# Performance work log

Measured on AMD Instinct MI355X. Metric: run time of the kernel, lower is better.

Reference implementation:

```python
import jax, jax.numpy as jnp
import numpy as np

N_HEAD = 16
THETA = 10000.0


def _freqs_cos_sin(head_dim, seq_len):
    # matches precompute_freqs_cis: freqs = 1/theta^(arange(0,dim,2)/dim), outer with t
    inv = 1.0 / (THETA ** (jnp.arange(0, head_dim, 2, dtype=jnp.float32) / head_dim))
    t = jnp.arange(seq_len, dtype=jnp.float32)
    ang = jnp.outer(t, inv)  # [L, head_dim//2]
    return jnp.cos(ang), jnp.sin(ang)


def _rope(x, cos, sin):
    # x: [B, H, L, D]; pairs are interleaved (view_as_complex on (..., D//2, 2))
    x1 = x[..., 0::2]
    x2 = x[..., 1::2]
    out_re = x1 * cos - x2 * sin
    out_im = x1 * sin + x2 * cos
    return jnp.stack([out_re, out_im], axis=-1).reshape(x.shape)


def setup_inputs() -> dict:
    key = jax.random.key(0)
    ks = jax.random.split(key, 11)
    B, L, D = 2, 2048, 1024
    s = 0.02
    return {
        "q": jax.random.normal(ks[0], (B, L, D), jnp.float32),
        "k": jax.random.normal(ks[1], (B, L, D), jnp.float32),
        "v": jax.random.normal(ks[2], (B, L, D), jnp.float32),
        "wq": jax.random.normal(ks[3], (D, D), jnp.float32) * s,
        "bq": jax.random.normal(ks[4], (D,), jnp.float32) * s,
        "wk": jax.random.normal(ks[5], (D, D), jnp.float32) * s,
        "bk": jax.random.normal(ks[6], (D,), jnp.float32) * s,
        "wv": jax.random.normal(ks[7], (D, D), jnp.float32) * s,
        "bv": jax.random.normal(ks[8], (D,), jnp.float32) * s,
        "wo": jax.random.normal(ks[9], (D, D), jnp.float32) * s,
        "bo": jax.random.normal(ks[10], (D,), jnp.float32) * s,
    }


def reference(q, k, v, wq, bq, wk, bk, wv, bv, wo, bo):
    B, L, D = q.shape
    Hd = D // N_HEAD
    # projections (nn.Linear: x @ W^T + b)
    qp = q @ wq.T + bq
    kp = k @ wk.T + bk
    vp = v @ wv.T + bv
    # split: [B, L, D] -> [B, H, L, Hd]
    def split(t):
        return t.reshape(B, L, N_HEAD, Hd).transpose(0, 2, 1, 3)
    qh, kh, vh = split(qp), split(kp), split(vp)
    cos, sin = _freqs_cos_sin(Hd, L)  # [L, Hd//2], broadcasts over B, H
    qh = _rope(qh, cos, sin)
    kh = _rope(kh, cos, sin)
    # scaled dot-product attention (no mask)
    scores = jnp.einsum("bhqd,bhkd->bhqk", qh, kh) / jnp.sqrt(jnp.float32(Hd))
    attn = jax.nn.softmax(scores, axis=-1)
    out = jnp.einsum("bhqk,bhkd->bhqd", attn, vh)
    # concat heads and output projection
    out = out.transpose(0, 2, 1, 3).reshape(B, L, D)
    return out @ wo.T + bo
```

## Files before the change

kernel.cpp:

```cpp
#include <hip/hip_runtime.h>
#include <hip/hip_bf16.h>
#include <math.h>

#define BB 2
#define LL 2048
#define DD 1024
#define NH 16
#define HD 64

typedef short v8s __attribute__((ext_vector_type(8)));
typedef float v4f __attribute__((ext_vector_type(4)));
typedef float v16f __attribute__((ext_vector_type(16)));

__device__ __forceinline__ float b2f(unsigned short b) {
  union { unsigned int u; float f; } c; c.u = ((unsigned int)b) << 16; return c.f;
}
__device__ __forceinline__ unsigned short f2b(float x) {
  union { float f; unsigned int u; } c; c.f = x;
  unsigned int u = c.u;
  u += 0x7fffu + ((u >> 16) & 1u);
  return (unsigned short)(u >> 16);
}
__device__ __forceinline__ unsigned int asu(float x) {
  union { float f; unsigned int u; } c; c.f = x; return c.u;
}
__device__ __forceinline__ unsigned int pk2(float lo, float hi) {
  return __builtin_amdgcn_perm(asu(hi), asu(lo), 0x07060302u);
}

#if defined(__has_builtin)
#if __has_builtin(__builtin_amdgcn_exp2f)
#define EXP2(x) __builtin_amdgcn_exp2f(x)
#else
#define EXP2(x) __expf((x) * 0.69314718056f)
#endif
#else
#define EXP2(x) __expf((x) * 0.69314718056f)
#endif

__device__ __forceinline__ void gload16(const void* g, void* l) {
  __builtin_amdgcn_global_load_lds(
      (const __attribute__((address_space(1))) void*)g,
      (__attribute__((address_space(3))) void*)l, 16, 0, 0);
}

#define VM_WAIT4 do { asm volatile("s_waitcnt vmcnt(4)" ::: "memory"); \
                      __builtin_amdgcn_sched_barrier(0); } while (0)
#define VM_WAIT2 do { asm volatile("s_waitcnt vmcnt(2)" ::: "memory"); \
                      __builtin_amdgcn_sched_barrier(0); } while (0)
#define VM_WAIT0 do { asm volatile("s_waitcnt vmcnt(0)" ::: "memory"); \
                      __builtin_amdgcn_sched_barrier(0); } while (0)
#define SBAR     do { __builtin_amdgcn_s_barrier(); \
                      __builtin_amdgcn_sched_barrier(0); } while (0)

struct CastArgs { const float* s[7]; unsigned short* d[7]; float* ct; float* st; };
__global__ void cast_all(CastArgs a) {
  int z = blockIdx.z;
  if (z == 16) {
    if (blockIdx.x >= 256) return;
    int id = blockIdx.x * blockDim.x + threadIdx.x;
    int t = id >> 5, i = id & 31;
    float inv = powf(10000.0f, -(float)(2 * i) / 64.0f);
    float ang = (float)t * inv;
    a.ct[id] = cosf(ang);
    a.st[id] = sinf(ang);
    return;
  }
  int t = (z < 12) ? (z >> 2) : (z - 9);
  int off = (z < 12) ? ((z & 3) << 18) : 0;
  int i = off + blockIdx.x * blockDim.x + threadIdx.x;
  float4 v = ((const float4*)a.s[t])[i];
  ushort4 o;
  o.x = f2b(v.x); o.y = f2b(v.y); o.z = f2b(v.z); o.w = f2b(v.w);
  ((ushort4*)a.d[t])[i] = o;
}

__device__ __forceinline__ size_t ring_src_off(int id, int row0, int Kd) {
  int sr = id >> 3, slot = id & 7;
  int g = slot ^ (sr & 7);
  int r = (sr << 1) | (g >> 2), c = g & 3;
  return (size_t)(row0 + r) * Kd + c * 8;
}
__device__ __forceinline__ int ring_frag_off(int row, int quad) {
  int sr = row >> 1;
  int slot = (((row & 1) << 2) | quad) ^ (sr & 7);
  return sr * 64 + slot * 8;
}

__device__ __forceinline__ void ring_gemm_core(
    const unsigned short* __restrict__ X, const unsigned short* __restrict__ W,
    unsigned short* LDS_, int bm0, int bn0, v4f acc[4][4]) {
  const int K = DD;
  const int tid = threadIdx.x;
  const int lane = tid & 63, wave = tid >> 6;
  const int quad = lane >> 4, l16 = lane & 15;
  const int wm = (wave >> 1) * 64, wn = (wave & 1) * 64;

  const unsigned short* aS0 = X + ring_src_off(tid, bm0, K);
  const unsigned short* aS1 = X + ring_src_off(256 + tid, bm0, K);
  const unsigned short* bS0 = W + ring_src_off(tid, bn0, K);
  const unsigned short* bS1 = W + ring_src_off(256 + tid, bn0, K);

  int aoff[4], boff[4];
#pragma unroll
  for (int i = 0; i < 4; ++i) {
    aoff[i] = ring_frag_off(wm + i * 16 + l16, quad);
    boff[i] = ring_frag_off(wn + i * 16 + l16, quad);
  }

  auto stage = [&](int q, int kofs) {
    unsigned short* Ab = &LDS_[q * 4096];
    unsigned short* Bb = &LDS_[12288 + q * 4096];
    gload16(aS0 + kofs, &Ab[tid * 8]);
    gload16(aS1 + kofs, &Ab[(256 + tid) * 8]);
    gload16(bS0 + kofs, &Bb[tid * 8]);
    gload16(bS1 + kofs, &Bb[(256 + tid) * 8]);
  };
  auto compute = [&](int q) {
    const unsigned short* Ab = &LDS_[q * 4096];
    const unsigned short* Bb = &LDS_[12288 + q * 4096];
    v8s a[4], b[4];
#pragma unroll
    for (int i = 0; i < 4; ++i) {
      a[i] = *(const v8s*)&Ab[aoff[i]];
      b[i] = *(const v8s*)&Bb[boff[i]];
    }
#pragma unroll
    for (int mi = 0; mi < 4; ++mi)
#pragma unroll
      for (int ni = 0; ni < 4; ++ni)
        acc[mi][ni] = __builtin_amdgcn_mfma_f32_16x16x32_bf16(a[mi], b[ni], acc[mi][ni], 0, 0, 0);
  };

  const int nt = K / 32;
  stage(0, 0);
  stage(1, 32);
  VM_WAIT4;
  SBAR;
  int cur = 0, s2 = 2, kofs = 64;
#pragma unroll 1
  for (int t = 0; t < nt - 2; ++t) {
    stage(s2, kofs);
    compute(cur);
    VM_WAIT4;
    SBAR;
    cur = (cur == 2) ? 0 : cur + 1;
    s2 = (s2 == 2) ? 0 : s2 + 1;
    kofs += 32;
  }
  compute(cur);
  VM_WAIT0;
  SBAR;
  cur = (cur == 2) ? 0 : cur + 1;
  compute(cur);
}

__global__ __launch_bounds__(256, 3) void gemm_qkv(
    const unsigned short* __restrict__ qb, const unsigned short* __restrict__ kb,
    const unsigned short* __restrict__ vb,
    const unsigned short* __restrict__ wqb, const unsigned short* __restrict__ wkb,
    const unsigned short* __restrict__ wvb,
    const float* __restrict__ bq, const float* __restrict__ bk,
    const float* __restrict__ bv_,
    unsigned short* __restrict__ qp, unsigned short* __restrict__ khh,
    unsigned short* __restrict__ vt,
    const float* __restrict__ ctab, const float* __restrict__ stab) {
  __shared__ __align__(16) unsigned short LDS_[24576];
  const int z = blockIdx.z;
  const unsigned short* X = (z == 0) ? qb : (z == 1) ? kb : vb;
  const unsigned short* W = (z == 0) ? wqb : (z == 1) ? wkb : wvb;
  const float* bias = (z == 0) ? bq : (z == 1) ? bk : bv_;
  const int N = DD;
  const int tid = threadIdx.x;
  const int lane = tid & 63, wave = tid >> 6;
  const int quad = lane >> 4, l16 = lane & 15;
  const int bm0 = blockIdx.x * 128;
  const int bn0 = blockIdx.y * 128;
  const int wm = (wave >> 1) * 64, wn = (wave & 1) * 64;

  const v4f vzero = {0.f, 0.f, 0.f, 0.f};
  v4f acc[4][4];
#pragma unroll
  for (int i = 0; i < 4; ++i)
#pragma unroll
    for (int j = 0; j < 4; ++j) acc[i][j] = vzero;

  ring_gemm_core(X, W, LDS_, bm0, bn0, acc);

  float bv[4];
#pragma unroll
  for (int ni = 0; ni < 4; ++ni) bv[ni] = bias[bn0 + wn + ni * 16 + l16];

  if (z < 2) {
    const float scl = (z == 0) ? 0.18033688f : 1.0f;
    const int h = (bn0 + wn) >> 6;
    const float sgn = (l16 & 1) ? 1.0f : -1.0f;
#pragma unroll
    for (int mi = 0; mi < 4; ++mi) {
#pragma unroll
      for (int r = 0; r < 4; ++r) {
        int row = bm0 + wm + mi * 16 + quad * 4 + r;
        int l = row & (LL - 1);
        int bidx = row >> 11;
        size_t baseq = (size_t)row * N + bn0 + wn + l16;
        size_t basek = ((size_t)(bidx * NH + h) * LL + l) * HD + l16;
#pragma unroll
        for (int ni = 0; ni < 4; ++ni) {
          int ii = (ni * 16 + l16) >> 1;
          float c = ctab[l * 32 + ii], s = stab[l * 32 + ii];
          float v = acc[mi][ni][r] + bv[ni];
          float vp = __shfl_xor(v, 1);
          float o = (v * c + sgn * (vp * s)) * scl;
          if (z == 0) qp[baseq + ni * 16] = f2b(o);
          else        khh[basek + ni * 16] = f2b(o);
        }
      }
    }
  } else {
    __syncthreads();
    unsigned short* T = LDS_;
#pragma unroll
    for (int mi = 0; mi < 4; ++mi)
#pragma unroll
      for (int r = 0; r < 4; ++r) {
        int tl = wm + mi * 16 + quad * 4 + r;
        int tlp = (tl & ~12) | ((tl & 4) << 1) | ((tl & 8) >> 1);
        int chunk = tlp >> 3, offw = tlp & 7;
#pragma unroll
        for (int ni = 0; ni < 4; ++ni) {
          int fl = wn + ni * 16 + l16;
          T[fl * 128 + ((chunk ^ (fl & 15)) * 8) + offw] =
              f2b(acc[mi][ni][r] + bv[ni]);
        }
      }
    __syncthreads();
    int fl = tid >> 1, half = tid & 1;
    int fg = bn0 + fl;
    int h2 = fg >> 6, d = fg & 63;
    int bidx = bm0 >> 11, l0 = bm0 & (LL - 1);
    unsigned short* dst =
        vt + (((size_t)(bidx * NH + h2) * HD + d) * LL) + l0 + half * 64;
#pragma unroll
    for (int i = 0; i < 8; ++i) {
      int chunk = half * 8 + i;
      int slot = chunk ^ (fl & 15);
      *(v8s*)(dst + i * 8) = *(const v8s*)&T[fl * 128 + slot * 8];
    }
  }
}

__global__ __launch_bounds__(256, 3) void gemm_out(
    const unsigned short* __restrict__ x, const unsigned short* __restrict__ w,
    const float* __restrict__ b, float* __restrict__ y) {
  __shared__ __align__(16) unsigned short LDS_[24576];
  const int N = DD;
  const int tid = threadIdx.x;
  const int lane = tid & 63, wave = tid >> 6;
  const int quad = lane >> 4, l16 = lane & 15;
  const int bm0 = blockIdx.x * 128;
  const int bn0 = blockIdx.y * 128;
  const int wm = (wave >> 1) * 64, wn = (wave & 1) * 64;

  const v4f vzero = {0.f, 0.f, 0.f, 0.f};
  v4f acc[4][4];
#pragma unroll
  for (int i = 0; i < 4; ++i)
#pragma unroll
    for (int j = 0; j < 4; ++j) acc[i][j] = vzero;

  ring_gemm_core(x, w, LDS_, bm0, bn0, acc);

  float bv[4];
#pragma unroll
  for (int ni = 0; ni < 4; ++ni) bv[ni] = b[bn0 + wn + ni * 16 + l16];
#pragma unroll
  for (int mi = 0; mi < 4; ++mi) {
#pragma unroll
    for (int r = 0; r < 4; ++r) {
      int row = bm0 + wm + mi * 16 + quad * 4 + r;
      size_t base = (size_t)row * N + bn0 + wn + l16;
#pragma unroll
      for (int ni = 0; ni < 4; ++ni)
        y[base + ni * 16] = acc[mi][ni][r] + bv[ni];
    }
  }
}

__global__ __launch_bounds__(256, 4) void flash_split(
    const unsigned short* __restrict__ qp,
    const unsigned short* __restrict__ kh,
    const unsigned short* __restrict__ vt,
    unsigned short* __restrict__ opart,
    float* __restrict__ lspart) {
  __shared__ __align__(16) unsigned short S_[12288];
  const int tid = threadIdx.x, wave = tid >> 6, lane = tid & 63;
  const int l32 = lane & 31, hf = lane >> 5;
  const int bh = blockIdx.x, b = bh >> 4, hd = bh & 15;
  const int qt = blockIdx.y, ks = blockIdx.z;
  const int q0 = qt * 128;
  const unsigned short* kbase = kh + (size_t)bh * LL * HD + (size_t)ks * 1024 * HD;
  const unsigned short* vbase = vt + (size_t)bh * HD * LL + ks * 1024;

  const int qrow = q0 + wave * 32 + l32;
  v8s qf[4];
  {
    const unsigned short* qsrc = qp + ((size_t)(b * LL + qrow) * DD + hd * HD);
#pragma unroll
    for (int ks2 = 0; ks2 < 4; ++ks2)
      qf[ks2] = *(const v8s*)(qsrc + ks2 * 16 + hf * 8);
  }

  const int rk = tid >> 3, sk = tid & 7;
  const int rv = tid >> 2, sv = tid & 3;
  const unsigned short* kS = kbase + (size_t)rk * HD + ((sk ^ (rk & 7)) * 8);
  const unsigned short* vS = vbase + (size_t)rv * LL + ((sv ^ (rv & 3)) * 8);

  v16f o0, o1;
#pragma unroll
  for (int i = 0; i < 16; ++i) { o0[i] = 0.0f; o1[i] = 0.0f; }
  float ls = 0.0f;

  auto stage = [&](int q, int t) {
    gload16(kS + t * 2048, &S_[q * 4096 + tid * 8]);
    gload16(vS + t * 32, &S_[q * 4096 + 2048 + tid * 8]);
  };

  auto compute = [&](int q) {
    const unsigned short* Ks = &S_[q * 4096];
    const unsigned short* Vs = Ks + 2048;
    v16f sc;
#pragma unroll
    for (int i = 0; i < 16; ++i) sc[i] = 0.0f;
#pragma unroll
    for (int ks2 = 0; ks2 < 4; ++ks2) {
      v8s kf = *(const v8s*)&Ks[l32 * 64 + (((ks2 * 2 + hf) ^ (l32 & 7)) * 8)];
      sc = __builtin_amdgcn_mfma_f32_32x32x16_bf16(kf, qf[ks2], sc, 0, 0, 0);
    }
    v16f e;
#pragma unroll
    for (int i = 0; i < 16; ++i) e[i] = EXP2(sc[i]);
    float t0 = (e[0] + e[1]) + (e[2] + e[3]);
    float t1 = (e[4] + e[5]) + (e[6] + e[7]);
    float t2 = (e[8] + e[9]) + (e[10] + e[11]);
    float t3 = (e[12] + e[13]) + (e[14] + e[15]);
    ls += (t0 + t1) + (t2 + t3);
    union { v8s v; unsigned int u[4]; } pb0, pb1;
#pragma unroll
    for (int a = 0; a < 4; ++a) {
      pb0.u[a] = pk2(e[2 * a], e[2 * a + 1]);
      pb1.u[a] = pk2(e[8 + 2 * a], e[8 + 2 * a + 1]);
    }
    int slot0 = (hf) ^ (l32 & 3);
    int slot1 = (2 + hf) ^ (l32 & 3);
    v8s vfa0 = *(const v8s*)&Vs[l32 * 32 + slot0 * 8];
    v8s vfb0 = *(const v8s*)&Vs[(32 + l32) * 32 + slot0 * 8];
    v8s vfa1 = *(const v8s*)&Vs[l32 * 32 + slot1 * 8];
    v8s vfb1 = *(const v8s*)&Vs[(32 + l32) * 32 + slot1 * 8];
    o0 = __builtin_amdgcn_mfma_f32_32x32x16_bf16(vfa0, pb0.v, o0, 0, 0, 0);
    o1 = __builtin_amdgcn_mfma_f32_32x32x16_bf16(vfb0, pb0.v, o1, 0, 0, 0);
    o0 = __builtin_amdgcn_mfma_f32_32x32x16_bf16(vfa1, pb1.v, o0, 0, 0, 0);
    o1 = __builtin_amdgcn_mfma_f32_32x32x16_bf16(vfb1, pb1.v, o1, 0, 0, 0);
  };

  const int nt = 32;
  stage(0, 0);
  stage(1, 1);
  VM_WAIT2;
  SBAR;
  int cur = 0, s2 = 2;
#pragma unroll 1
  for (int t = 0; t < nt - 2; ++t) {
    stage(s2, t + 2);
    compute(cur);
    VM_WAIT2;
    SBAR;
    cur = (cur == 2) ? 0 : cur + 1;
    s2 = (s2 == 2) ? 0 : s2 + 1;
  }
  compute(cur);
  VM_WAIT0;
  SBAR;
  cur = (cur == 2) ? 0 : cur + 1;
  compute(cur);

  const int blk4 = ((bh * 16 + qt) * 2 + ks) * 4 + wave;
  lspart[blk4 * 64 + lane] = ls;
  unsigned short* ob = opart + (size_t)blk4 * 2048;
#pragma unroll
  for (int r = 0; r < 16; ++r) {
    ob[r * 64 + lane] = f2b(o0[r]);
    ob[(16 + r) * 64 + lane] = f2b(o1[r]);
  }
}

__global__ __launch_bounds__(256) void flash_combine(
    const unsigned short* __restrict__ opart, const float* __restrict__ lspart,
    unsigned short* __restrict__ attn) {
  __shared__ __align__(16) unsigned short W_[8192];
  const int tid = threadIdx.x, wave = tid >> 6, lane = tid & 63;
  const int l32 = lane & 31, hf = lane >> 5;
  const int bh = blockIdx.x, b = bh >> 4, hd = bh & 15;
  const int qt = blockIdx.y, q0 = qt * 128;

  const int p0 = ((bh * 16 + qt) * 2 + 0) * 4 + wave;
  const int p1 = p0 + 4;
  float lsv = lspart[p0 * 64 + lane] + lspart[p1 * 64 + lane];
  lsv += __shfl_xor(lsv, 32);
  float inv = 1.0f / lsv;

  const unsigned short* oa = opart + (size_t)p0 * 2048;
  const unsigned short* ob = opart + (size_t)p1 * 2048;
  unsigned short* Wt = W_ + wave * 2048;
#pragma unroll
  for (int dt = 0; dt < 2; ++dt)
#pragma unroll
    for (int r = 0; r < 16; ++r) {
      int idx = (dt * 16 + r) * 64 + lane;
      float val = (b2f(oa[idx]) + b2f(ob[idx])) * inv;
      int dl = (r & 3) + 8 * (r >> 2) + 4 * hf;
      int d = dt * 32 + dl;
      int chunk = d >> 3, offw = d & 7;
      int slot = chunk ^ (l32 & 7);
      Wt[l32 * 64 + slot * 8 + offw] = f2b(val);
    }
#pragma unroll
  for (int i = 0; i < 4; ++i) {
    int qr = lane >> 1;
    int chunk = (lane & 1) * 4 + i;
    int slot = chunk ^ (qr & 7);
    v8s dv = *(const v8s*)&Wt[qr * 64 + slot * 8];
    int token = q0 + wave * 32 + qr;
    *(v8s*)(attn + ((size_t)(b * LL + token) * DD) + hd * HD + chunk * 8) = dv;
  }
}

extern "C" void kernel_launch(void* const* d_in, const int* in_sizes, int n_in,
                              void* d_out, int out_size, void* d_ws, size_t ws_size,
                              hipStream_t stream) {
  const float* q  = (const float*)d_in[0];
  const float* k  = (const float*)d_in[1];
  const float* v  = (const float*)d_in[2];
  const float* wq = (const float*)d_in[3];
  const float* bq = (const float*)d_in[4];
  const float* wk = (const float*)d_in[5];
  const float* bk = (const float*)d_in[6];
  const float* wv = (const float*)d_in[7];
  const float* bv = (const float*)d_in[8];
  const float* wo = (const float*)d_in[9];
  const float* bo = (const float*)d_in[10];
  float* out = (float*)d_out;

  size_t off = 0;
  char* wsb = (char*)d_ws;
  auto take = [&](size_t n) { void* p = wsb + off; off += n; return p; };
  const size_t SZT = (size_t)BB * LL * DD * 2;
  const size_t SZW = (size_t)DD * DD * 2;
  unsigned short* qb   = (unsigned short*)take(SZT);
  unsigned short* kb   = (unsigned short*)take(SZT);
  unsigned short* vb   = (unsigned short*)take(SZT);
  unsigned short* wqb  = (unsigned short*)take(SZW);
  unsigned short* wkb  = (unsigned short*)take(SZW);
  unsigned short* wvb  = (unsigned short*)take(SZW);
  unsigned short* wob  = (unsigned short*)take(SZW);
  unsigned short* qp   = (unsigned short*)take(SZT);
  unsigned short* khh  = (unsigned short*)take(SZT);
  unsigned short* vtt  = (unsigned short*)take(SZT);
  unsigned short* attn = (unsigned short*)take(SZT);
  float* ctab = (float*)take((size_t)LL * 32 * 4);
  float* stab = (float*)take((size_t)LL * 32 * 4);

  unsigned short* opart = qb;
  float* lspart = (float*)wqb;

  CastArgs ca;
  ca.s[0] = q;  ca.s[1] = k;  ca.s[2] = v;  ca.s[3] = wq;
  ca.s[4] = wk; ca.s[5] = wv; ca.s[6] = wo;
  ca.d[0] = qb;  ca.d[1] = kb;  ca.d[2] = vb;  ca.d[3] = wqb;
  ca.d[4] = wkb; ca.d[5] = wvb; ca.d[6] = wob;
  ca.ct = ctab; ca.st = stab;
  cast_all<<<dim3(1024, 1, 17), 256, 0, stream>>>(ca);

  gemm_qkv<<<dim3(BB * LL / 128, DD / 128, 3), 256, 0, stream>>>(
      qb, kb, vb, wqb, wkb, wvb, bq, bk, bv, qp, khh, vtt, ctab, stab);

  flash_split<<<dim3(BB * NH, LL / 128, 2), 256, 0, stream>>>(
      qp, khh, vtt, opart, lspart);

  flash_combine<<<dim3(BB * NH, LL / 128), 256, 0, stream>>>(
      opart, lspart, attn);

  gemm_out<<<dim3(BB * LL / 128, DD / 128, 1), 256, 0, stream>>>(attn, wob, bo, out);
}
```

Before: 220.4 us.

## Process two 32-row query tiles per wave to reuse K/V LDS fragments

Each wave in the flash attention kernel now handles 64 query rows as two 32-row groups instead of 32. The K and V fragments read from LDS are reused across both groups, and the V staging layout and read offsets are rearranged. The grid is halved along the query dimension and the combine kernel is updated to match. The aim is to halve K/V global and LDS traffic per query row. The cost is roughly double the accumulator registers, lower occupancy (launch bounds drop from 4 to 2), and fewer blocks to fill the GPU.

```diff
diff --git a/kernel.cpp b/kernel.cpp
--- a/kernel.cpp
+++ b/kernel.cpp
@@ -286,7 +286,7 @@
   }
 }
 
-__global__ __launch_bounds__(256, 4) void flash_split(
+__global__ __launch_bounds__(256, 2) void flash_split(
     const unsigned short* __restrict__ qp,
     const unsigned short* __restrict__ kh,
     const unsigned short* __restrict__ vt,
@@ -297,69 +297,111 @@
   const int l32 = lane & 31, hf = lane >> 5;
   const int bh = blockIdx.x, b = bh >> 4, hd = bh & 15;
   const int qt = blockIdx.y, ks = blockIdx.z;
-  const int q0 = qt * 128;
+  const int qbase = qt * 256 + wave * 64;
   const unsigned short* kbase = kh + (size_t)bh * LL * HD + (size_t)ks * 1024 * HD;
   const unsigned short* vbase = vt + (size_t)bh * HD * LL + ks * 1024;
 
-  const int qrow = q0 + wave * 32 + l32;
-  v8s qf[4];
+  v8s qfA[4], qfB[4];
   {
-    const unsigned short* qsrc = qp + ((size_t)(b * LL + qrow) * DD + hd * HD);
-#pragma unroll
-    for (int ks2 = 0; ks2 < 4; ++ks2)
-      qf[ks2] = *(const v8s*)(qsrc + ks2 * 16 + hf * 8);
+    const unsigned short* qa = qp + ((size_t)(b * LL + qbase + l32) * DD + hd * HD);
+    const unsigned short* qbp = qp + ((size_t)(b * LL + qbase + 32 + l32) * DD + hd * HD);
+#pragma unroll
+    for (int ks2 = 0; ks2 < 4; ++ks2) {
+      qfA[ks2] = *(const v8s*)(qa + ks2 * 16 + hf * 8);
+      qfB[ks2] = *(const v8s*)(qbp + ks2 * 16 + hf * 8);
+    }
   }
 
   const int rk = tid >> 3, sk = tid & 7;
-  const int rv = tid >> 2, sv = tid & 3;
   const unsigned short* kS = kbase + (size_t)rk * HD + ((sk ^ (rk & 7)) * 8);
-  const unsigned short* vS = vbase + (size_t)rv * LL + ((sv ^ (rv & 3)) * 8);
-
-  v16f o0, o1;
-#pragma unroll
-  for (int i = 0; i < 16; ++i) { o0[i] = 0.0f; o1[i] = 0.0f; }
-  float ls = 0.0f;
+  const int srv = tid >> 3, slv = tid & 7;
+  const int gv = slv ^ (srv & 7);
+  const int dv_ = srv * 2 + (gv >> 2), cv = gv & 3;
+  const unsigned short* vS = vbase + (size_t)dv_ * LL + cv * 8;
+
+  v16f oA0, oA1, oB0, oB1;
+#pragma unroll
+  for (int i = 0; i < 16; ++i) { oA0[i] = 0.f; oA1[i] = 0.f; oB0[i] = 0.f; oB1[i] = 0.f; }
+  float lsA = 0.0f, lsB = 0.0f;
 
   auto stage = [&](int q, int t) {
     gload16(kS + t * 2048, &S_[q * 4096 + tid * 8]);
     gload16(vS + t * 32, &S_[q * 4096 + 2048 + tid * 8]);
   };
 
+  int voff[2][2];
+#pragma unroll
+  for (int k16 = 0; k16 < 2; ++k16) {
+    int c = k16 * 2 + hf;
+    int srA = l32 >> 1;
+    int srB = 16 + (l32 >> 1);
+    voff[k16][0] = srA * 64 + ((((l32 & 1) * 4 + c) ^ (srA & 7)) * 8);
+    voff[k16][1] = srB * 64 + ((((l32 & 1) * 4 + c) ^ (srB & 7)) * 8);
+  }
+  int koff[4];
+#pragma unroll
+  for (int ks2 = 0; ks2 < 4; ++ks2)
+    koff[ks2] = l32 * 64 + (((ks2 * 2 + hf) ^ (l32 & 7)) * 8);
+
   auto compute = [&](int q) {
     const unsigned short* Ks = &S_[q * 4096];
     const unsigned short* Vs = Ks + 2048;
+    v8s kf[4];
     v16f sc;
 #pragma unroll
     for (int i = 0; i < 16; ++i) sc[i] = 0.0f;
 #pragma unroll
     for (int ks2 = 0; ks2 < 4; ++ks2) {
-      v8s kf = *(const v8s*)&Ks[l32 * 64 + (((ks2 * 2 + hf) ^ (l32 & 7)) * 8)];
-      sc = __builtin_amdgcn_mfma_f32_32x32x16_bf16(kf, qf[ks2], sc, 0, 0, 0);
+      kf[ks2] = *(const v8s*)&Ks[koff[ks2]];
+      sc = __builtin_amdgcn_mfma_f32_32x32x16_bf16(kf[ks2], qfA[ks2], sc, 0, 0, 0);
     }
     v16f e;
 #pragma unroll
     for (int i = 0; i < 16; ++i) e[i] = EXP2(sc[i]);
-    float t0 = (e[0] + e[1]) + (e[2] + e[3]);
-    float t1 = (e[4] + e[5]) + (e[6] + e[7]);
-    float t2 = (e[8] + e[9]) + (e[10] + e[11]);
-    float t3 = (e[12] + e[13]) + (e[14] + e[15]);
-    ls += (t0 + t1) + (t2 + t3);
+    {
+      float t0 = (e[0] + e[1]) + (e[2] + e[3]);
+      float t1 = (e[4] + e[5]) + (e[6] + e[7]);
+      float t2 = (e[8] + e[9]) + (e[10] + e[11]);
+      float t3 = (e[12] + e[13]) + (e[14] + e[15]);
+      lsA += (t0 + t1) + (t2 + t3);
+    }
     union { v8s v; unsigned int u[4]; } pb0, pb1;
 #pragma unroll
     for (int a = 0; a < 4; ++a) {
       pb0.u[a] = pk2(e[2 * a], e[2 * a + 1]);
       pb1.u[a] = pk2(e[8 + 2 * a], e[8 + 2 * a + 1]);
     }
-    int slot0 = (hf) ^ (l32 & 3);
-    int slot1 = (2 + hf) ^ (l32 & 3);
-    v8s vfa0 = *(const v8s*)&Vs[l32 * 32 + slot0 * 8];
-    v8s vfb0 = *(const v8s*)&Vs[(32 + l32) * 32 + slot0 * 8];
-    v8s vfa1 = *(const v8s*)&Vs[l32 * 32 + slot1 * 8];
-    v8s vfb1 = *(const v8s*)&Vs[(32 + l32) * 32 + slot1 * 8];
-    o0 = __builtin_amdgcn_mfma_f32_32x32x16_bf16(vfa0, pb0.v, o0, 0, 0, 0);
-    o1 = __builtin_amdgcn_mfma_f32_32x32x16_bf16(vfb0, pb0.v, o1, 0, 0, 0);
-    o0 = __builtin_amdgcn_mfma_f32_32x32x16_bf16(vfa1, pb1.v, o0, 0, 0, 0);
-    o1 = __builtin_amdgcn_mfma_f32_32x32x16_bf16(vfb1, pb1.v, o1, 0, 0, 0);
+    v8s vf00 = *(const v8s*)&Vs[voff[0][0]];
+    v8s vf01 = *(const v8s*)&Vs[voff[0][1]];
+    v8s vf10 = *(const v8s*)&Vs[voff[1][0]];
+    v8s vf11 = *(const v8s*)&Vs[voff[1][1]];
+    oA0 = __builtin_amdgcn_mfma_f32_32x32x16_bf16(vf00, pb0.v, oA0, 0, 0, 0);
+    oA1 = __builtin_amdgcn_mfma_f32_32x32x16_bf16(vf01, pb0.v, oA1, 0, 0, 0);
+    oA0 = __builtin_amdgcn_mfma_f32_32x32x16_bf16(vf10, pb1.v, oA0, 0, 0, 0);
+    oA1 = __builtin_amdgcn_mfma_f32_32x32x16_bf16(vf11, pb1.v, oA1, 0, 0, 0);
+#pragma unroll
+    for (int i = 0; i < 16; ++i) sc[i] = 0.0f;
+#pragma unroll
+    for (int ks2 = 0; ks2 < 4; ++ks2)
+      sc = __builtin_amdgcn_mfma_f32_32x32x16_bf16(kf[ks2], qfB[ks2], sc, 0, 0, 0);
+#pragma unroll
+    for (int i = 0; i < 16; ++i) e[i] = EXP2(sc[i]);
+    {
+      float t0 = (e[0] + e[1]) + (e[2] + e[3]);
+      float t1 = (e[4] + e[5]) + (e[6] + e[7]);
+      float t2 = (e[8] + e[9]) + (e[10] + e[11]);
+      float t3 = (e[12] + e[13]) + (e[14] + e[15]);
+      lsB += (t0 + t1) + (t2 + t3);
+    }
+#pragma unroll
+    for (int a = 0; a < 4; ++a) {
+      pb0.u[a] = pk2(e[2 * a], e[2 * a + 1]);
+      pb1.u[a] = pk2(e[8 + 2 * a], e[8 + 2 * a + 1]);
+    }
+    oB0 = __builtin_amdgcn_mfma_f32_32x32x16_bf16(vf00, pb0.v, oB0, 0, 0, 0);
+    oB1 = __builtin_amdgcn_mfma_f32_32x32x16_bf16(vf01, pb0.v, oB1, 0, 0, 0);
+    oB0 = __builtin_amdgcn_mfma_f32_32x32x16_bf16(vf10, pb1.v, oB0, 0, 0, 0);
+    oB1 = __builtin_amdgcn_mfma_f32_32x32x16_bf16(vf11, pb1.v, oB1, 0, 0, 0);
   };
 
   const int nt = 32;
@@ -383,53 +425,63 @@
   cur = (cur == 2) ? 0 : cur + 1;
   compute(cur);
 
-  const int blk4 = ((bh * 16 + qt) * 2 + ks) * 4 + wave;
-  lspart[blk4 * 64 + lane] = ls;
-  unsigned short* ob = opart + (size_t)blk4 * 2048;
+  const int blk4 = ((bh * 8 + qt) * 2 + ks) * 4 + wave;
+  lspart[blk4 * 128 + lane] = lsA;
+  lspart[blk4 * 128 + 64 + lane] = lsB;
+  unsigned short* ob = opart + (size_t)blk4 * 4096;
 #pragma unroll
   for (int r = 0; r < 16; ++r) {
-    ob[r * 64 + lane] = f2b(o0[r]);
-    ob[(16 + r) * 64 + lane] = f2b(o1[r]);
+    ob[(0 * 16 + r) * 64 + lane] = f2b(oA0[r]);
+    ob[(1 * 16 + r) * 64 + lane] = f2b(oA1[r]);
+    ob[(2 * 16 + r) * 64 + lane] = f2b(oB0[r]);
+    ob[(3 * 16 + r) * 64 + lane] = f2b(oB1[r]);
   }
 }
 
 __global__ __launch_bounds__(256) void flash_combine(
     const unsigned short* __restrict__ opart, const float* __restrict__ lspart,
     unsigned short* __restrict__ attn) {
-  __shared__ __align__(16) unsigned short W_[8192];
+  __shared__ __align__(16) unsigned short W_[16384];
   const int tid = threadIdx.x, wave = tid >> 6, lane = tid & 63;
   const int l32 = lane & 31, hf = lane >> 5;
   const int bh = blockIdx.x, b = bh >> 4, hd = bh & 15;
-  const int qt = blockIdx.y, q0 = qt * 128;
-
-  const int p0 = ((bh * 16 + qt) * 2 + 0) * 4 + wave;
+  const int qt = blockIdx.y, q0 = qt * 256;
+
+  const int p0 = ((bh * 8 + qt) * 2 + 0) * 4 + wave;
   const int p1 = p0 + 4;
-  float lsv = lspart[p0 * 64 + lane] + lspart[p1 * 64 + lane];
-  lsv += __shfl_xor(lsv, 32);
-  float inv = 1.0f / lsv;
-
-  const unsigned short* oa = opart + (size_t)p0 * 2048;
-  const unsigned short* ob = opart + (size_t)p1 * 2048;
-  unsigned short* Wt = W_ + wave * 2048;
-#pragma unroll
-  for (int dt = 0; dt < 2; ++dt)
+  float lsvA = lspart[p0 * 128 + lane] + lspart[p1 * 128 + lane];
+  lsvA += __shfl_xor(lsvA, 32);
+  float invA = 1.0f / lsvA;
+  float lsvB = lspart[p0 * 128 + 64 + lane] + lspart[p1 * 128 + 64 + lane];
+  lsvB += __shfl_xor(lsvB, 32);
+  float invB = 1.0f / lsvB;
+
+  const unsigned short* oa = opart + (size_t)p0 * 4096;
+  const unsigned short* obp = opart + (size_t)p1 * 4096;
+  unsigned short* Wt = W_ + wave * 4096;
+#pragma unroll
+  for (int set = 0; set < 4; ++set) {
+    int g = set >> 1, dt = set & 1;
+    float inv = g ? invB : invA;
+    int q64 = g * 32 + l32;
 #pragma unroll
     for (int r = 0; r < 16; ++r) {
-      int idx = (dt * 16 + r) * 64 + lane;
-      float val = (b2f(oa[idx]) + b2f(ob[idx])) * inv;
+      int idx = (set * 16 + r) * 64 + lane;
+      float val = (b2f(oa[idx]) + b2f(obp[idx])) * inv;
       int dl = (r & 3) + 8 * (r >> 2) + 4 * hf;
       int d = dt * 32 + dl;
       int chunk = d >> 3, offw = d & 7;
-      int slot = chunk ^ (l32 & 7);
-      Wt[l32 * 64 + slot * 8 + offw] = f2b(val);
-    }
-#pragma unroll
-  for (int i = 0; i < 4; ++i) {
-    int qr = lane >> 1;
-    int chunk = (lane & 1) * 4 + i;
+      int slot = chunk ^ (q64 & 7);
+      Wt[q64 * 64 + slot * 8 + offw] = f2b(val);
+    }
+  }
+#pragma unroll
+  for (int i = 0; i < 8; ++i) {
+    int qr = (i & 1) * 32 + (lane >> 1);
+    int chunk = (lane & 1) * 4 + (i >> 1);
     int slot = chunk ^ (qr & 7);
     v8s dv = *(const v8s*)&Wt[qr * 64 + slot * 8];
-    int token = q0 + wave * 32 + qr;
+    int token = q0 + wave * 64 + qr;
     *(v8s*)(attn + ((size_t)(b * LL + token) * DD) + hd * HD + chunk * 8) = dv;
   }
 }
@@ -483,10 +535,10 @@
   gemm_qkv<<<dim3(BB * LL / 128, DD / 128, 3), 256, 0, stream>>>(
       qb, kb, vb, wqb, wkb, wvb, bq, bk, bv, qp, khh, vtt, ctab, stab);
 
-  flash_split<<<dim3(BB * NH, LL / 128, 2), 256, 0, stream>>>(
+  flash_split<<<dim3(BB * NH, LL / 256, 2), 256, 0, stream>>>(
       qp, khh, vtt, opart, lspart);
 
-  flash_combine<<<dim3(BB * NH, LL / 128), 256, 0, stream>>>(
+  flash_combine<<<dim3(BB * NH, LL / 256), 256, 0, stream>>>(
       opart, lspart, attn);
 
   gemm_out<<<dim3(BB * LL / 128, DD / 128, 1), 256, 0, stream>>>(attn, wob, bo, out);
```

Result: faster. 215.9 us (-2.1%).
